# Kernel optimization log

Measured on AMD Instinct MI355X. Metric: run time of the kernel, lower is better.

Reference implementation:

```python
import jax, jax.numpy as jnp
import numpy as np

MARGIN = 5.0  # margin_between_clusters


def setup_inputs() -> dict:
    key = jax.random.key(0)
    k1, k2, k3 = jax.random.split(key, 3)
    N, D, K = 262144, 128, 64
    embeddings = jax.random.normal(k1, (N, D), dtype=jnp.float32)
    cluster_labels = jax.random.randint(k2, (N,), 0, K, dtype=jnp.int64)
    centroids = jax.random.normal(k3, (K, D), dtype=jnp.float32)
    return {"embeddings": embeddings, "cluster_labels": cluster_labels, "centroids": centroids}


def reference(embeddings, cluster_labels, centroids):
    # Assumes all K clusters are present in cluster_labels (true w.h.p. for N >> K),
    # matching number_cluster = len(unique(labels)) in the original.
    N, d = embeddings.shape
    K = centroids.shape[0]
    labels = cluster_labels.astype(jnp.int32)

    x2 = jnp.sum(embeddings * embeddings, axis=1, keepdims=True)        # [N,1]
    c2 = jnp.sum(centroids * centroids, axis=1)[None, :]                # [1,K]
    d2 = jnp.maximum(x2 + c2 - 2.0 * (embeddings @ centroids.T), 0.0)  # [N,K]
    dist = jnp.sqrt(d2)

    rows = jnp.arange(N)
    own_d = dist[rows, labels]                 # distance to own centroid
    counts = jax.ops.segment_sum(jnp.ones((N,), embeddings.dtype), labels, num_segments=K)
    safe_counts = jnp.maximum(counts, 1.0)

    # attraction: per cluster, mean of squared distance to own centroid
    attr_per_cluster = jax.ops.segment_sum(own_d * own_d, labels, num_segments=K) / safe_counts
    attraction_loss = jnp.sum(jnp.where(counts > 0, attr_per_cluster, 0.0))

    # repulsion: per cluster, mean over (points_in_cluster x other_centroids) of relu((m - d)^2)
    rep = jax.nn.relu((MARGIN - dist) ** 2)    # [N,K]
    row_other = (jnp.sum(rep, axis=1) - rep[rows, labels]) / (K - 1)
    rep_per_cluster = jax.ops.segment_sum(row_other, labels, num_segments=K) / safe_counts
    repulsion_loss = jnp.sum(jnp.where(counts > 0, rep_per_cluster, 0.0))

    return (attraction_loss + repulsion_loss) / K
```

## Files before the change

### kernel.cpp

```cpp
#include <hip/hip_runtime.h>


constexpr int N = 262144;
constexpr int D = 128;
constexpr int K = 64;

constexpr int GRID = 512;
constexpr int TPW  = 4;
constexpr int PANEL = 32 * 32;

typedef __bf16 bf16x4 __attribute__((ext_vector_type(4)));
typedef __bf16 bf16x8 __attribute__((ext_vector_type(8)));
typedef float  f32x16 __attribute__((ext_vector_type(16)));

__global__ __launch_bounds__(256, 2) void dcl_main(
    const float* __restrict__ emb,
    const int*   __restrict__ labels,
    const float* __restrict__ cent,
    float* __restrict__ g_attr,
    float* __restrict__ g_rep,
    int*   __restrict__ g_cnt)
{
    __shared__ bf16x8 sA[2 * 8 * 64];
    __shared__ __align__(16) bf16x4 sPanel[4 * PANEL];
    __shared__ float  s_c2[K];
    __shared__ __align__(16) float sC2i0[2][16];
    __shared__ __align__(16) float sC2i1[2][16];
    __shared__ float  s_attr[K];
    __shared__ float  s_rep[K];
    __shared__ int    s_cnt[K];

    const int tid  = threadIdx.x;
    const int wave = tid >> 6;
    const int lane = tid & 63;
    const int l31  = lane & 31;
    const int h    = lane >> 5;

    const int g     = blockIdx.x * 4 + wave;
    const int base  = g * TPW;

    float4 bufA[16], bufB[16];
    {
        const float4* src = (const float4*)emb + (size_t)base * 1024 + lane;
        #pragma unroll
        for (int q = 0; q < 16; ++q) bufA[q] = src[q * 64];
    }
    int lbl[TPW];
    #pragma unroll
    for (int t = 0; t < TPW; ++t) lbl[t] = labels[(base + t) * 32 + l31];

    #pragma unroll
    for (int e = tid; e < 2 * 8 * 64; e += 256) {
        const int t = e >> 9, s = (e >> 6) & 7, l = e & 63;
        const int c  = t * 32 + (l & 31);
        const int d0 = 16 * s + 8 * (l >> 5);
        const float4 f0 = *(const float4*)(cent + c * D + d0);
        const float4 f1 = *(const float4*)(cent + c * D + d0 + 4);
        bf16x8 v;
        v[0] = (__bf16)f0.x; v[1] = (__bf16)f0.y; v[2] = (__bf16)f0.z; v[3] = (__bf16)f0.w;
        v[4] = (__bf16)f1.x; v[5] = (__bf16)f1.y; v[6] = (__bf16)f1.z; v[7] = (__bf16)f1.w;
        sA[e] = v;
    }
    if (tid < K) {
        const float4* cp = (const float4*)(cent + tid * D);
        float sa = 0.f, sb = 0.f;
        #pragma unroll
        for (int q = 0; q < D / 8; ++q) {
            const float4 f = cp[2 * q];
            const float4 gg = cp[2 * q + 1];
            sa = fmaf(f.x, f.x, sa); sa = fmaf(f.y, f.y, sa);
            sa = fmaf(f.z, f.z, sa); sa = fmaf(f.w, f.w, sa);
            sb = fmaf(gg.x, gg.x, sb); sb = fmaf(gg.y, gg.y, sb);
            sb = fmaf(gg.z, gg.z, sb); sb = fmaf(gg.w, gg.w, sb);
        }
        s_c2[tid] = sa + sb;
        s_attr[tid] = 0.f; s_rep[tid] = 0.f; s_cnt[tid] = 0;
    }
    __syncthreads();
    if (tid < 32) {
        const int hh = tid >> 4, r = tid & 15;
        const int rb = (r & 3) + 8 * (r >> 2) + 4 * hh;
        sC2i0[hh][r] = -0.5f * s_c2[rb];
        sC2i1[hh][r] = -0.5f * s_c2[rb + 32];
    }
    __syncthreads();

    bf16x4* panel = sPanel + wave * PANEL;

    #pragma unroll
    for (int t = 0; t < TPW; ++t) {
        float4* cur = (t & 1) ? bufB : bufA;
        float4* nxt = (t & 1) ? bufA : bufB;

        #pragma unroll
        for (int q = 0; q < 16; ++q) {
            bf16x4 v;
            v[0] = (__bf16)cur[q].x; v[1] = (__bf16)cur[q].y;
            v[2] = (__bf16)cur[q].z; v[3] = (__bf16)cur[q].w;
            const int n = 2 * q + h;
            const int sw = ((((l31 >> 1) ^ (n & 15)) << 1) | (l31 & 1));
            panel[32 * n + sw] = v;
        }

        if (t + 1 < TPW) {
            const float4* src = (const float4*)emb + (size_t)(base + t + 1) * 1024 + lane;
            #pragma unroll
            for (int q = 0; q < 16; ++q) nxt[q] = src[q * 64];
        }
        __builtin_amdgcn_sched_barrier(0);

        f32x16 acc0, acc1;
        {
            const float4* p0 = (const float4*)&sC2i0[h][0];
            const float4* p1 = (const float4*)&sC2i1[h][0];
            #pragma unroll
            for (int w = 0; w < 4; ++w) {
                ((float4*)&acc0)[w] = p0[w];
                ((float4*)&acc1)[w] = p1[w];
            }
        }

        __builtin_amdgcn_s_setprio(1);
        float x2A = 0.f, x2B = 0.f;
        #pragma unroll
        for (int s = 0; s < 8; ++s) {
            const bf16x8 b = *(const bf16x8*)&panel[32 * l31 + 2 * ((2 * s + h) ^ (l31 & 15))];
            {
                const float e0 = (float)b[0], e1 = (float)b[1], e2 = (float)b[2], e3 = (float)b[3];
                const float e4 = (float)b[4], e5 = (float)b[5], e6 = (float)b[6], e7 = (float)b[7];
                float p0 = e0 * e0; p0 = fmaf(e1, e1, p0); p0 = fmaf(e2, e2, p0); p0 = fmaf(e3, e3, p0);
                float p1 = e4 * e4; p1 = fmaf(e5, e5, p1); p1 = fmaf(e6, e6, p1); p1 = fmaf(e7, e7, p1);
                x2A += p0; x2B += p1;
            }
            const bf16x8 a0 = sA[s * 64 + lane];
            const bf16x8 a1 = sA[(8 + s) * 64 + lane];
            acc0 = __builtin_amdgcn_mfma_f32_32x32x16_bf16(a0, b, acc0, 0, 0, 0);
            acc1 = __builtin_amdgcn_mfma_f32_32x32x16_bf16(a1, b, acc1, 0, 0, 0);
        }
        __builtin_amdgcn_s_setprio(0);

        const float x2p = x2A + x2B;
        const float x2 = x2p + __shfl_xor(x2p, 32);
        const int li = lbl[t];

        float s1a = 0.f, s1b = 0.f, s2a = 0.f, s2b = 0.f, own = 0.f;
        #pragma unroll
        for (int r = 0; r < 16; ++r) {
            const int rbase = (r & 3) + 8 * (r >> 2) + 4 * h;
            {
                float d2 = fmaf(-2.f, acc0[r], x2);
                d2 = fmaxf(d2, 0.f);
                const float dd = __builtin_amdgcn_sqrtf(d2);
                s1a += dd; s2a += d2;
                if (rbase == li) own += d2;
            }
            {
                float d2 = fmaf(-2.f, acc1[r], x2);
                d2 = fmaxf(d2, 0.f);
                const float dd = __builtin_amdgcn_sqrtf(d2);
                s1b += dd; s2b += d2;
                if (rbase + 32 == li) own += d2;
            }
        }
        float s1 = s1a + s1b, s2 = s2a + s2b;
        s1  += __shfl_xor(s1, 32);
        s2  += __shfl_xor(s2, 32);
        own += __shfl_xor(own, 32);

        if (lane < 32) {
            const float down = __builtin_amdgcn_sqrtf(own);
            const float own_term = fmaf(-10.f, down, 25.f) + own;
            const float row_other = (25.f * K - 10.f * s1 + s2 - own_term) * (1.f / (K - 1));
            atomicAdd(&s_attr[li], own);
            atomicAdd(&s_rep[li], row_other);
            atomicAdd(&s_cnt[li], 1);
        }
    }

    __syncthreads();
    if (tid < K) {
        const int rep8 = (blockIdx.x & 7) * K;
        atomicAdd(&g_attr[rep8 + tid], s_attr[tid]);
        atomicAdd(&g_rep[rep8 + tid], s_rep[tid]);
        atomicAdd(&g_cnt[rep8 + tid], s_cnt[tid]);
    }
}

__global__ void dcl_finish(const float* __restrict__ g_attr,
                           const float* __restrict__ g_rep,
                           const int*   __restrict__ g_cnt,
                           float* __restrict__ out)
{
    const int k = threadIdx.x;
    float a = 0.f, r = 0.f;
    int   c = 0;
    #pragma unroll
    for (int j = 0; j < 8; ++j) {
        a += g_attr[j * K + k];
        r += g_rep[j * K + k];
        c += g_cnt[j * K + k];
    }
    float v = (c > 0) ? (a + r) / (float)c : 0.f;
    #pragma unroll
    for (int off = 32; off > 0; off >>= 1) v += __shfl_down(v, off);
    if (k == 0) out[0] = v * (1.f / K);
}

extern "C" void kernel_launch(void* const* d_in, const int* in_sizes, int n_in,
                              void* d_out, int out_size, void* d_ws, size_t ws_size,
                              hipStream_t stream) {
    const float* emb    = (const float*)d_in[0];
    const int*   labels = (const int*)d_in[1];
    const float* cent   = (const float*)d_in[2];
    float* out = (float*)d_out;

    float* g_attr = (float*)d_ws;
    float* g_rep  = g_attr + 8 * K;
    int*   g_cnt  = (int*)(g_rep + 8 * K);

    hipMemsetAsync(d_ws, 0, 3 * 8 * K * sizeof(float), stream);
    dcl_main<<<GRID, 256, 0, stream>>>(emb, labels, cent, g_attr, g_rep, g_cnt);
    dcl_finish<<<1, 64, 0, stream>>>(g_attr, g_rep, g_cnt, out);
}
```

Before: 198.8 us.

## Load embedding rows directly into MFMA B-operand registers, drop LDS panel

```diff
diff --git a/kernel.cpp b/kernel.cpp
--- a/kernel.cpp
+++ b/kernel.cpp
@@ -5,15 +5,12 @@
 constexpr int D = 128;
 constexpr int K = 64;
 
-constexpr int GRID = 512;
-constexpr int TPW  = 4;
-constexpr int PANEL = 32 * 32;
-
-typedef __bf16 bf16x4 __attribute__((ext_vector_type(4)));
+constexpr int GRID = 2048;
+
 typedef __bf16 bf16x8 __attribute__((ext_vector_type(8)));
 typedef float  f32x16 __attribute__((ext_vector_type(16)));
 
-__global__ __launch_bounds__(256, 2) void dcl_main(
+__global__ __launch_bounds__(256, 4) void dcl_main(
     const float* __restrict__ emb,
     const int*   __restrict__ labels,
     const float* __restrict__ cent,
@@ -22,7 +19,6 @@
     int*   __restrict__ g_cnt)
 {
     __shared__ bf16x8 sA[2 * 8 * 64];
-    __shared__ __align__(16) bf16x4 sPanel[4 * PANEL];
     __shared__ float  s_c2[K];
     __shared__ __align__(16) float sC2i0[2][16];
     __shared__ __align__(16) float sC2i1[2][16];
@@ -36,18 +32,17 @@
     const int l31  = lane & 31;
     const int h    = lane >> 5;
 
-    const int g     = blockIdx.x * 4 + wave;
-    const int base  = g * TPW;
-
-    float4 bufA[16], bufB[16];
-    {
-        const float4* src = (const float4*)emb + (size_t)base * 1024 + lane;
-        #pragma unroll
-        for (int q = 0; q < 16; ++q) bufA[q] = src[q * 64];
-    }
-    int lbl[TPW];
-    #pragma unroll
-    for (int t = 0; t < TPW; ++t) lbl[t] = labels[(base + t) * 32 + l31];
+    const int tile = blockIdx.x * 4 + wave;
+    const int row  = tile * 32 + l31;
+
+    const float4* row4 = (const float4*)emb + (size_t)row * 32 + 2 * h;
+    float4 f[16];
+    #pragma unroll
+    for (int s = 0; s < 8; ++s) {
+        f[2 * s]     = row4[4 * s];
+        f[2 * s + 1] = row4[4 * s + 1];
+    }
+    const int li = labels[row];
 
     #pragma unroll
     for (int e = tid; e < 2 * 8 * 64; e += 256) {
@@ -66,10 +61,10 @@
         float sa = 0.f, sb = 0.f;
         #pragma unroll
         for (int q = 0; q < D / 8; ++q) {
-            const float4 f = cp[2 * q];
+            const float4 fq = cp[2 * q];
             const float4 gg = cp[2 * q + 1];
-            sa = fmaf(f.x, f.x, sa); sa = fmaf(f.y, f.y, sa);
-            sa = fmaf(f.z, f.z, sa); sa = fmaf(f.w, f.w, sa);
+            sa = fmaf(fq.x, fq.x, sa); sa = fmaf(fq.y, fq.y, sa);
+            sa = fmaf(fq.z, fq.z, sa); sa = fmaf(fq.w, fq.w, sa);
             sb = fmaf(gg.x, gg.x, sb); sb = fmaf(gg.y, gg.y, sb);
             sb = fmaf(gg.z, gg.z, sb); sb = fmaf(gg.w, gg.w, sb);
         }
@@ -85,96 +80,77 @@
     }
     __syncthreads();
 
-    bf16x4* panel = sPanel + wave * PANEL;
-
-    #pragma unroll
-    for (int t = 0; t < TPW; ++t) {
-        float4* cur = (t & 1) ? bufB : bufA;
-        float4* nxt = (t & 1) ? bufA : bufB;
-
+    bf16x8 b[8];
+    float x2A = 0.f, x2B = 0.f;
+    #pragma unroll
+    for (int s = 0; s < 8; ++s) {
+        const float4 f0 = f[2 * s], f1 = f[2 * s + 1];
+        bf16x8 v;
+        v[0] = (__bf16)f0.x; v[1] = (__bf16)f0.y; v[2] = (__bf16)f0.z; v[3] = (__bf16)f0.w;
+        v[4] = (__bf16)f1.x; v[5] = (__bf16)f1.y; v[6] = (__bf16)f1.z; v[7] = (__bf16)f1.w;
+        b[s] = v;
+        const float e0 = (float)v[0], e1 = (float)v[1], e2 = (float)v[2], e3 = (float)v[3];
+        const float e4 = (float)v[4], e5 = (float)v[5], e6 = (float)v[6], e7 = (float)v[7];
+        float p0 = e0 * e0; p0 = fmaf(e1, e1, p0); p0 = fmaf(e2, e2, p0); p0 = fmaf(e3, e3, p0);
+        float p1 = e4 * e4; p1 = fmaf(e5, e5, p1); p1 = fmaf(e6, e6, p1); p1 = fmaf(e7, e7, p1);
+        x2A += p0; x2B += p1;
+    }
+
+    f32x16 acc0, acc1;
+    {
+        const float4* p0 = (const float4*)&sC2i0[h][0];
+        const float4* p1 = (const float4*)&sC2i1[h][0];
         #pragma unroll
-        for (int q = 0; q < 16; ++q) {
-            bf16x4 v;
-            v[0] = (__bf16)cur[q].x; v[1] = (__bf16)cur[q].y;
-            v[2] = (__bf16)cur[q].z; v[3] = (__bf16)cur[q].w;
-            const int n = 2 * q + h;
-            const int sw = ((((l31 >> 1) ^ (n & 15)) << 1) | (l31 & 1));
-            panel[32 * n + sw] = v;
-        }
-
-        if (t + 1 < TPW) {
-            const float4* src = (const float4*)emb + (size_t)(base + t + 1) * 1024 + lane;
-            #pragma unroll
-            for (int q = 0; q < 16; ++q) nxt[q] = src[q * 64];
-        }
-        __builtin_amdgcn_sched_barrier(0);
-
-        f32x16 acc0, acc1;
+        for (int w = 0; w < 4; ++w) {
+            ((float4*)&acc0)[w] = p0[w];
+            ((float4*)&acc1)[w] = p1[w];
+        }
+    }
+
+    __builtin_amdgcn_s_setprio(1);
+    #pragma unroll
+    for (int s = 0; s < 8; ++s) {
+        const bf16x8 a0 = sA[s * 64 + lane];
+        const bf16x8 a1 = sA[(8 + s) * 64 + lane];
+        acc0 = __builtin_amdgcn_mfma_f32_32x32x16_bf16(a0, b[s], acc0, 0, 0, 0);
+        acc1 = __builtin_amdgcn_mfma_f32_32x32x16_bf16(a1, b[s], acc1, 0, 0, 0);
+    }
+    __builtin_amdgcn_s_setprio(0);
+
+    const float x2p = x2A + x2B;
+    const float x2 = x2p + __shfl_xor(x2p, 32);
+
+    float s1a = 0.f, s1b = 0.f, s2a = 0.f, s2b = 0.f, own = 0.f;
+    #pragma unroll
+    for (int r = 0; r < 16; ++r) {
+        const int rbase = (r & 3) + 8 * (r >> 2) + 4 * h;
         {
-            const float4* p0 = (const float4*)&sC2i0[h][0];
-            const float4* p1 = (const float4*)&sC2i1[h][0];
-            #pragma unroll
-            for (int w = 0; w < 4; ++w) {
-                ((float4*)&acc0)[w] = p0[w];
-                ((float4*)&acc1)[w] = p1[w];
-            }
-        }
-
-        __builtin_amdgcn_s_setprio(1);
-        float x2A = 0.f, x2B = 0.f;
-        #pragma unroll
-        for (int s = 0; s < 8; ++s) {
-            const bf16x8 b = *(const bf16x8*)&panel[32 * l31 + 2 * ((2 * s + h) ^ (l31 & 15))];
-            {
-                const float e0 = (float)b[0], e1 = (float)b[1], e2 = (float)b[2], e3 = (float)b[3];
-                const float e4 = (float)b[4], e5 = (float)b[5], e6 = (float)b[6], e7 = (float)b[7];
-                float p0 = e0 * e0; p0 = fmaf(e1, e1, p0); p0 = fmaf(e2, e2, p0); p0 = fmaf(e3, e3, p0);
-                float p1 = e4 * e4; p1 = fmaf(e5, e5, p1); p1 = fmaf(e6, e6, p1); p1 = fmaf(e7, e7, p1);
-                x2A += p0; x2B += p1;
-            }
-            const bf16x8 a0 = sA[s * 64 + lane];
-            const bf16x8 a1 = sA[(8 + s) * 64 + lane];
-            acc0 = __builtin_amdgcn_mfma_f32_32x32x16_bf16(a0, b, acc0, 0, 0, 0);
-            acc1 = __builtin_amdgcn_mfma_f32_32x32x16_bf16(a1, b, acc1, 0, 0, 0);
-        }
-        __builtin_amdgcn_s_setprio(0);
-
-        const float x2p = x2A + x2B;
-        const float x2 = x2p + __shfl_xor(x2p, 32);
-        const int li = lbl[t];
-
-        float s1a = 0.f, s1b = 0.f, s2a = 0.f, s2b = 0.f, own = 0.f;
-        #pragma unroll
-        for (int r = 0; r < 16; ++r) {
-            const int rbase = (r & 3) + 8 * (r >> 2) + 4 * h;
-            {
-                float d2 = fmaf(-2.f, acc0[r], x2);
-                d2 = fmaxf(d2, 0.f);
-                const float dd = __builtin_amdgcn_sqrtf(d2);
-                s1a += dd; s2a += d2;
-                if (rbase == li) own += d2;
-            }
-            {
-                float d2 = fmaf(-2.f, acc1[r], x2);
-                d2 = fmaxf(d2, 0.f);
-                const float dd = __builtin_amdgcn_sqrtf(d2);
-                s1b += dd; s2b += d2;
-                if (rbase + 32 == li) own += d2;
-            }
-        }
-        float s1 = s1a + s1b, s2 = s2a + s2b;
-        s1  += __shfl_xor(s1, 32);
-        s2  += __shfl_xor(s2, 32);
-        own += __shfl_xor(own, 32);
-
-        if (lane < 32) {
-            const float down = __builtin_amdgcn_sqrtf(own);
-            const float own_term = fmaf(-10.f, down, 25.f) + own;
-            const float row_other = (25.f * K - 10.f * s1 + s2 - own_term) * (1.f / (K - 1));
-            atomicAdd(&s_attr[li], own);
-            atomicAdd(&s_rep[li], row_other);
-            atomicAdd(&s_cnt[li], 1);
-        }
+            float d2 = fmaf(-2.f, acc0[r], x2);
+            d2 = fmaxf(d2, 0.f);
+            const float dd = __builtin_amdgcn_sqrtf(d2);
+            s1a += dd; s2a += d2;
+            if (rbase == li) own += d2;
+        }
+        {
+            float d2 = fmaf(-2.f, acc1[r], x2);
+            d2 = fmaxf(d2, 0.f);
+            const float dd = __builtin_amdgcn_sqrtf(d2);
+            s1b += dd; s2b += d2;
+            if (rbase + 32 == li) own += d2;
+        }
+    }
+    float s1 = s1a + s1b, s2 = s2a + s2b;
+    s1  += __shfl_xor(s1, 32);
+    s2  += __shfl_xor(s2, 32);
+    own += __shfl_xor(own, 32);
+
+    if (lane < 32) {
+        const float down = __builtin_amdgcn_sqrtf(own);
+        const float own_term = fmaf(-10.f, down, 25.f) + own;
+        const float row_other = (25.f * K - 10.f * s1 + s2 - own_term) * (1.f / (K - 1));
+        atomicAdd(&s_attr[li], own);
+        atomicAdd(&s_rep[li], row_other);
+        atomicAdd(&s_cnt[li], 1);
     }
 
     __syncthreads();
```

Result: slower. 206.5 us (+3.9%).
